# Performance work log

Hardware: AMD Instinct MI355X
Metric: run time of the kernel (lower is better)

## Reference

```python
import jax, jax.numpy as jnp
import numpy as np

B, N, M = 262144, 8, 4  # batch, state dim, measurement dim


def _psd(key, b, d, scale):
    # SPD matrix: A @ A^T / d + 0.1*I  (keeps inverse well-conditioned)
    A = jax.random.normal(key, (b, d, d), dtype=jnp.float32) * scale
    return A @ A.swapaxes(-1, -2) / d + 0.1 * jnp.eye(d, dtype=jnp.float32)


def setup_inputs() -> dict:
    key = jax.random.key(0)
    kF, kH, kS, kQ, kR = jax.random.split(key, 5)
    F = jax.random.normal(kF, (B, N, N), dtype=jnp.float32) * 0.3 + jnp.eye(N, dtype=jnp.float32)
    H = jax.random.normal(kH, (B, M, N), dtype=jnp.float32) * 0.5
    Sigma_previous = _psd(kS, B, N, 1.0)
    Q = _psd(kQ, B, N, 0.3)
    R = _psd(kR, B, M, 0.3)
    return {"F": F, "H": H, "Sigma_previous": Sigma_previous, "Q": Q, "R": R}


def reference(F, H, Sigma_previous, Q, R):
    T = lambda x: x.swapaxes(-1, -2)
    # predicted state covariance: Sigma = F Sigma_prev F^T + Q        [B,N,N]
    Sigma = F @ Sigma_previous @ T(F) + Q
    # innovation covariance: S = H Sigma H^T + R                      [B,M,M]
    S = H @ Sigma @ T(H) + R
    # Kalman gain: KG = Sigma H^T S^{-1}                              [B,N,M]
    P12 = Sigma @ T(H)
    KG = P12 @ jnp.linalg.inv(S)
    return KG
```

## Files before the change

### kernel.cpp

```cpp
#include <hip/hip_runtime.h>


#define NBB 64
#define THREADS 128

__device__ __forceinline__ void gl_lds16(const float* src, float4* dst) {
    __builtin_amdgcn_global_load_lds(
        (const __attribute__((address_space(1))) unsigned int*)src,
        (__attribute__((address_space(3))) unsigned int*)dst,
        16, 0, 0);
}

__global__ __launch_bounds__(THREADS) void kalman_gain_kernel(
    const float* __restrict__ Fg, const float* __restrict__ Hg,
    const float* __restrict__ Spg, const float* __restrict__ Qg,
    const float* __restrict__ Rg, float* __restrict__ out, int nb)
{
    __shared__ float4 smem4[2816];

    const int tid  = threadIdx.x;
    const int wid  = tid >> 6;
    const int lane = tid & 63;
    const int b0   = blockIdx.x * NBB;

    for (int r = wid; r < 16; r += 2) {
        int s = (r << 6) | lane;
        int b = s >> 4, j = s & 15, k = j ^ (b & 15);
        gl_lds16(Fg + (size_t)(b0 + b) * 64 + k * 4, smem4 + (r << 6));
    }
    for (int r = wid; r < 16; r += 2) {
        int s = (r << 6) | lane;
        int b = s >> 4, j = s & 15, k = j ^ (b & 15);
        gl_lds16(Spg + (size_t)(b0 + b) * 64 + k * 4, smem4 + 1024 + (r << 6));
    }
    for (int r = wid; r < 8; r += 2) {
        int s = (r << 6) | lane;
        int b = s >> 3, j = s & 7, k = j ^ (b & 7);
        gl_lds16(Hg + (size_t)(b0 + b) * 32 + k * 4, smem4 + 2048 + (r << 6));
    }
    for (int r = wid; r < 4; r += 2) {
        int s = (r << 6) | lane;
        int b = s >> 2, j = s & 3, k = j ^ (b & 3);
        gl_lds16(Rg + (size_t)(b0 + b) * 16 + k * 4, smem4 + 2560 + (r << 6));
    }
    asm volatile("s_waitcnt vmcnt(0)" ::: "memory");
    __syncthreads();

    const int b_loc = tid >> 1;
    const int p     = tid & 1;
    const int bm15  = b_loc & 15;
    const int bm7   = b_loc & 7;

    float hs[16];
    #pragma unroll
    for (int j = 0; j < 4; ++j) {
        float4 v = smem4[2048 + b_loc * 8 + ((2 * j + p) ^ bm7)];
        hs[j*4+0] = v.x; hs[j*4+1] = v.y; hs[j*4+2] = v.z; hs[j*4+3] = v.w;
    }

    float fr[32];
    #pragma unroll
    for (int il = 0; il < 4; ++il) {
        #pragma unroll
        for (int hh = 0; hh < 2; ++hh) {
            int k = 8 * p + 2 * il + hh;
            float4 v = smem4[b_loc * 16 + (k ^ bm15)];
            fr[il*8 + hh*4 + 0] = v.x; fr[il*8 + hh*4 + 1] = v.y;
            fr[il*8 + hh*4 + 2] = v.z; fr[il*8 + hh*4 + 3] = v.w;
        }
    }

    __syncthreads();

    for (int r = wid; r < 16; r += 2) {
        int s = (r << 6) | lane;
        int b = s >> 4, j = s & 15, k = j ^ (b & 15);
        gl_lds16(Qg + (size_t)(b0 + b) * 64 + k * 4, smem4 + (r << 6));
    }

    float u[32];
    #pragma unroll
    for (int x = 0; x < 32; ++x) u[x] = 0.f;
    #pragma unroll
    for (int il = 0; il < 4; ++il)
        #pragma unroll
        for (int k = 0; k < 8; ++k)
            #pragma unroll
            for (int j = 0; j < 4; ++j)
                u[k*4+j] += hs[j*4+il] * fr[il*8+k];
    #pragma unroll
    for (int x = 0; x < 32; ++x) u[x] += __shfl_xor(u[x], 1, 64);

    float G[32];
    #pragma unroll
    for (int x = 0; x < 32; ++x) G[x] = 0.f;
    #pragma unroll
    for (int k = 0; k < 8; ++k) {
        float4 s0 = smem4[1024 + b_loc * 16 + ((2*k    ) ^ bm15)];
        float4 s1 = smem4[1024 + b_loc * 16 + ((2*k + 1) ^ bm15)];
        float sp[8] = {s0.x,s0.y,s0.z,s0.w, s1.x,s1.y,s1.z,s1.w};
        #pragma unroll
        for (int il = 0; il < 4; ++il)
            #pragma unroll
            for (int c = 0; c < 8; ++c)
                G[il*8+c] += fr[il*8+k] * sp[c];
    }

    float A[16];
    #pragma unroll
    for (int il = 0; il < 4; ++il)
        #pragma unroll
        for (int j = 0; j < 4; ++j) {
            float acc = 0.f;
            #pragma unroll
            for (int k = 0; k < 8; ++k)
                acc += G[il*8+k] * u[k*4+j];
            A[il*4+j] = acc;
        }

    asm volatile("s_waitcnt vmcnt(0)" ::: "memory");
    __syncthreads();

    float qo[32];
    #pragma unroll
    for (int il = 0; il < 4; ++il) {
        #pragma unroll
        for (int hh = 0; hh < 2; ++hh) {
            int k = 8 * p + 2 * il + hh;
            float4 v = smem4[b_loc * 16 + (k ^ bm15)];
            qo[il*8 + hh*4 + 0] = v.x; qo[il*8 + hh*4 + 1] = v.y;
            qo[il*8 + hh*4 + 2] = v.z; qo[il*8 + hh*4 + 3] = v.w;
        }
    }
    #pragma unroll
    for (int j = 0; j < 4; ++j) {
        float4 h0 = smem4[2048 + b_loc * 8 + ((2*j    ) ^ bm7)];
        float4 h1 = smem4[2048 + b_loc * 8 + ((2*j + 1) ^ bm7)];
        float hrow[8] = {h0.x,h0.y,h0.z,h0.w, h1.x,h1.y,h1.z,h1.w};
        #pragma unroll
        for (int il = 0; il < 4; ++il) {
            float acc = 0.f;
            #pragma unroll
            for (int k = 0; k < 8; ++k)
                acc += qo[il*8+k] * hrow[k];
            A[il*4+j] += acc;
        }
    }

    float s[16];
    #pragma unroll
    for (int pi = 0; pi < 4; ++pi)
        #pragma unroll
        for (int q = 0; q < 4; ++q) {
            float acc = 0.f;
            #pragma unroll
            for (int il = 0; il < 4; ++il)
                acc += hs[pi*4+il] * A[il*4+q];
            s[pi*4+q] = acc;
        }
    #pragma unroll
    for (int x = 0; x < 16; ++x) s[x] += __shfl_xor(s[x], 1, 64);
    #pragma unroll
    for (int pi = 0; pi < 4; ++pi) {
        float4 v = smem4[2560 + b_loc * 4 + (pi ^ (b_loc & 3))];
        s[pi*4+0] += v.x; s[pi*4+1] += v.y; s[pi*4+2] += v.z; s[pi*4+3] += v.w;
    }

    float is[16] = {1.f,0.f,0.f,0.f, 0.f,1.f,0.f,0.f, 0.f,0.f,1.f,0.f, 0.f,0.f,0.f,1.f};
    #pragma unroll
    for (int c = 0; c < 4; ++c) {
        float pinv = 1.0f / s[c*4+c];
        #pragma unroll
        for (int k = 0; k < 4; ++k) { s[c*4+k] *= pinv; is[c*4+k] *= pinv; }
        #pragma unroll
        for (int r = 0; r < 4; ++r) {
            if (r != c) {
                float fac = s[r*4+c];
                #pragma unroll
                for (int k = 0; k < 4; ++k) {
                    s[r*4+k]  -= fac * s[c*4+k];
                    is[r*4+k] -= fac * is[c*4+k];
                }
            }
        }
    }

    float4* outg = reinterpret_cast<float4*>(out) + (size_t)(b0 + b_loc) * 8 + p * 4;
    #pragma unroll
    for (int il = 0; il < 4; ++il) {
        float4 o;
        o.x = A[il*4+0]*is[0] + A[il*4+1]*is[4] + A[il*4+2]*is[8]  + A[il*4+3]*is[12];
        o.y = A[il*4+0]*is[1] + A[il*4+1]*is[5] + A[il*4+2]*is[9]  + A[il*4+3]*is[13];
        o.z = A[il*4+0]*is[2] + A[il*4+1]*is[6] + A[il*4+2]*is[10] + A[il*4+3]*is[14];
        o.w = A[il*4+0]*is[3] + A[il*4+1]*is[7] + A[il*4+2]*is[11] + A[il*4+3]*is[15];
        outg[il] = o;
    }
}

extern "C" void kernel_launch(void* const* d_in, const int* in_sizes, int n_in,
                              void* d_out, int out_size, void* d_ws, size_t ws_size,
                              hipStream_t stream) {
    const float* F  = (const float*)d_in[0];
    const float* H  = (const float*)d_in[1];
    const float* Sp = (const float*)d_in[2];
    const float* Q  = (const float*)d_in[3];
    const float* R  = (const float*)d_in[4];
    float* out = (float*)d_out;

    int nb = in_sizes[0] / 64;
    int blocks = nb / NBB;
    kalman_gain_kernel<<<blocks, THREADS, 0, stream>>>(F, H, Sp, Q, R, out, nb);
}
```

Baseline: 54.45 us.

## Stage loads with partial vmcnt waits and load R directly to registers

Reorders the async global-to-LDS loads so F and H land first, then Sigma_prev. Partial s_waitcnt plus barriers let the first H/F compute start while Sigma_prev is still loading. The Q load is issued after the u computation and overlaps the G computation. R is now read straight from global into registers instead of through LDS, which shrinks shared memory. This relies on vmcnt counting being exact per wave, so any extra global loads added by the compiler could break the partial-wait logic.

Measured after the change: 63.94 us. 17.4% more time.

```diff
diff --git a/kernel.cpp b/kernel.cpp
--- a/kernel.cpp
+++ b/kernel.cpp
@@ -3,6 +3,12 @@
 
 #define NBB 64
 #define THREADS 128
+
+#define WAIT_BAR(N) do {                                        \
+    asm volatile("s_waitcnt vmcnt(" #N ")" ::: "memory");       \
+    __builtin_amdgcn_s_barrier();                               \
+    __builtin_amdgcn_sched_barrier(0);                          \
+} while (0)
 
 __device__ __forceinline__ void gl_lds16(const float* src, float4* dst) {
     __builtin_amdgcn_global_load_lds(
@@ -16,35 +22,36 @@
     const float* __restrict__ Spg, const float* __restrict__ Qg,
     const float* __restrict__ Rg, float* __restrict__ out, int nb)
 {
-    __shared__ float4 smem4[2816];
+    __shared__ float4 smem4[2560];
 
     const int tid  = threadIdx.x;
     const int wid  = tid >> 6;
     const int lane = tid & 63;
     const int b0   = blockIdx.x * NBB;
 
-    for (int r = wid; r < 16; r += 2) {
-        int s = (r << 6) | lane;
+    #pragma unroll
+    for (int r = 0; r < 8; ++r) {
+        int rr = 2 * r + wid;
+        int s = (rr << 6) | lane;
         int b = s >> 4, j = s & 15, k = j ^ (b & 15);
-        gl_lds16(Fg + (size_t)(b0 + b) * 64 + k * 4, smem4 + (r << 6));
-    }
-    for (int r = wid; r < 16; r += 2) {
-        int s = (r << 6) | lane;
+        gl_lds16(Fg + (size_t)(b0 + b) * 64 + k * 4, smem4 + (rr << 6));
+    }
+    #pragma unroll
+    for (int r = 0; r < 4; ++r) {
+        int rr = 2 * r + wid;
+        int s = (rr << 6) | lane;
+        int b = s >> 3, j = s & 7, k = j ^ (b & 7);
+        gl_lds16(Hg + (size_t)(b0 + b) * 32 + k * 4, smem4 + 2048 + (rr << 6));
+    }
+    #pragma unroll
+    for (int r = 0; r < 8; ++r) {
+        int rr = 2 * r + wid;
+        int s = (rr << 6) | lane;
         int b = s >> 4, j = s & 15, k = j ^ (b & 15);
-        gl_lds16(Spg + (size_t)(b0 + b) * 64 + k * 4, smem4 + 1024 + (r << 6));
-    }
-    for (int r = wid; r < 8; r += 2) {
-        int s = (r << 6) | lane;
-        int b = s >> 3, j = s & 7, k = j ^ (b & 7);
-        gl_lds16(Hg + (size_t)(b0 + b) * 32 + k * 4, smem4 + 2048 + (r << 6));
-    }
-    for (int r = wid; r < 4; r += 2) {
-        int s = (r << 6) | lane;
-        int b = s >> 2, j = s & 3, k = j ^ (b & 3);
-        gl_lds16(Rg + (size_t)(b0 + b) * 16 + k * 4, smem4 + 2560 + (r << 6));
-    }
-    asm volatile("s_waitcnt vmcnt(0)" ::: "memory");
-    __syncthreads();
+        gl_lds16(Spg + (size_t)(b0 + b) * 64 + k * 4, smem4 + 1024 + (rr << 6));
+    }
+
+    WAIT_BAR(8);
 
     const int b_loc = tid >> 1;
     const int p     = tid & 1;
@@ -70,14 +77,6 @@
         }
     }
 
-    __syncthreads();
-
-    for (int r = wid; r < 16; r += 2) {
-        int s = (r << 6) | lane;
-        int b = s >> 4, j = s & 15, k = j ^ (b & 15);
-        gl_lds16(Qg + (size_t)(b0 + b) * 64 + k * 4, smem4 + (r << 6));
-    }
-
     float u[32];
     #pragma unroll
     for (int x = 0; x < 32; ++x) u[x] = 0.f;
@@ -90,6 +89,16 @@
                 u[k*4+j] += hs[j*4+il] * fr[il*8+k];
     #pragma unroll
     for (int x = 0; x < 32; ++x) u[x] += __shfl_xor(u[x], 1, 64);
+
+    WAIT_BAR(4);
+
+    #pragma unroll
+    for (int r = 0; r < 8; ++r) {
+        int rr = 2 * r + wid;
+        int s = (rr << 6) | lane;
+        int b = s >> 4, j = s & 15, k = j ^ (b & 15);
+        gl_lds16(Qg + (size_t)(b0 + b) * 64 + k * 4, smem4 + (rr << 6));
+    }
 
     float G[32];
     #pragma unroll
@@ -118,8 +127,10 @@
             A[il*4+j] = acc;
         }
 
-    asm volatile("s_waitcnt vmcnt(0)" ::: "memory");
-    __syncthreads();
+    const float4* R4g = reinterpret_cast<const float4*>(Rg) + (size_t)(b0 + b_loc) * 4;
+    float4 rr0 = R4g[0], rr1 = R4g[1], rr2 = R4g[2], rr3 = R4g[3];
+
+    WAIT_BAR(0);
 
     float qo[32];
     #pragma unroll
@@ -160,11 +171,10 @@
         }
     #pragma unroll
     for (int x = 0; x < 16; ++x) s[x] += __shfl_xor(s[x], 1, 64);
-    #pragma unroll
-    for (int pi = 0; pi < 4; ++pi) {
-        float4 v = smem4[2560 + b_loc * 4 + (pi ^ (b_loc & 3))];
-        s[pi*4+0] += v.x; s[pi*4+1] += v.y; s[pi*4+2] += v.z; s[pi*4+3] += v.w;
-    }
+    s[0]  += rr0.x; s[1]  += rr0.y; s[2]  += rr0.z; s[3]  += rr0.w;
+    s[4]  += rr1.x; s[5]  += rr1.y; s[6]  += rr1.z; s[7]  += rr1.w;
+    s[8]  += rr2.x; s[9]  += rr2.y; s[10] += rr2.z; s[11] += rr2.w;
+    s[12] += rr3.x; s[13] += rr3.y; s[14] += rr3.z; s[15] += rr3.w;
 
     float is[16] = {1.f,0.f,0.f,0.f, 0.f,1.f,0.f,0.f, 0.f,0.f,1.f,0.f, 0.f,0.f,0.f,1.f};
     #pragma unroll
```
